# Kernel tuning notes

Measured on AMD Instinct MI355X. Metric: run time of the kernel, lower is better.

## Reference

```python
import jax, jax.numpy as jnp
import numpy as np

N_NODES = 100000
N_EDGES = 1600000
IN_DIM = 128
EMB_DIM = 128
NUM_EDGE_EMB = 4
LN_EPS = 1e-5


def setup_inputs() -> dict:
    key = jax.random.key(0)
    ks = jax.random.split(key, 8)
    x = jax.random.normal(ks[0], (N_NODES, IN_DIM), dtype=jnp.float32)
    edge_index = jax.random.randint(ks[1], (2, N_EDGES), 0, N_NODES, dtype=jnp.int64)
    edge_attr = jax.random.randint(ks[2], (N_EDGES,), 0, NUM_EDGE_EMB, dtype=jnp.int64)
    # learned params
    edge_emb = jax.random.normal(ks[3], (NUM_EDGE_EMB, IN_DIM), dtype=jnp.float32)
    eps = jnp.zeros((), dtype=jnp.float32)  # GINEConv train_eps init 0
    s1 = 1.0 / np.sqrt(IN_DIM)
    W1 = jax.random.uniform(ks[4], (IN_DIM, EMB_DIM), jnp.float32, -s1, s1)
    b1 = jnp.zeros((EMB_DIM,), jnp.float32)
    ln_g = jnp.ones((EMB_DIM,), jnp.float32)
    ln_b = jnp.zeros((EMB_DIM,), jnp.float32)
    s2 = 1.0 / np.sqrt(EMB_DIM)
    W2 = jax.random.uniform(ks[5], (EMB_DIM, EMB_DIM), jnp.float32, -s2, s2)
    b2 = jnp.zeros((EMB_DIM,), jnp.float32)
    return {"x": x, "edge_index": edge_index, "edge_attr": edge_attr,
            "edge_emb": edge_emb, "eps": eps, "W1": W1, "b1": b1,
            "ln_g": ln_g, "ln_b": ln_b, "W2": W2, "b2": b2}


def reference(x, edge_index, edge_attr, edge_emb, eps, W1, b1, ln_g, ln_b, W2, b2):
    src, dst = edge_index[0], edge_index[1]
    # message: relu(x_j + e_ji), gathered per edge [E, D]
    msg = jax.nn.relu(x[src] + edge_emb[edge_attr])
    # scatter-add into destination nodes [N, D]
    agg = jax.ops.segment_sum(msg, dst, num_segments=x.shape[0])
    h = (1.0 + eps) * x + agg
    # MLP: Linear -> LayerNorm -> ReLU -> Linear
    h1 = h @ W1 + b1
    mu = jnp.mean(h1, axis=-1, keepdims=True)
    var = jnp.var(h1, axis=-1, keepdims=True)
    h1 = (h1 - mu) * jax.lax.rsqrt(var + LN_EPS) * ln_g + ln_b
    h1 = jax.nn.relu(h1)
    return h1 @ W2 + b2
```

## Files before the change

### kernel.cpp

```cpp
#include <hip/hip_runtime.h>
#include <hip/hip_fp16.h>

#define N_NODES 100000
#define N_EDGES 1600000
#define DIM 128
#define NBUK 782
#define EPB 4096
#define NBLK 391
#define NCNT (NBUK * NBLK)
#define NSC 299
#define CAPB 2720
#define CAPH 1536
#define EPT 11

typedef __attribute__((ext_vector_type(4))) float f32x4;
typedef _Float16 h2 __attribute__((ext_vector_type(2)));
typedef _Float16 h8v __attribute__((ext_vector_type(8)));

__device__ __forceinline__ unsigned short f2h16(float f) {
    return __half_as_ushort(__float2half(f));
}

__global__ __launch_bounds__(256) void hist2_conv(
    const int* __restrict__ ei, int* __restrict__ cnts,
    const float* __restrict__ x, ushort* __restrict__ xh, int do_conv)
{
    __shared__ int cnt[NBUK];
    for (int i = threadIdx.x; i < NBUK; i += 256) cnt[i] = 0;

    if (do_conv) {
        for (int i = blockIdx.x * 256 + threadIdx.x; i < N_NODES * DIM / 4;
             i += NBLK * 256) {
            float4 v = ((const float4*)x)[i];
            ushort4 o;
            o.x = f2h16(v.x);
            o.y = f2h16(v.y);
            o.z = f2h16(v.z);
            o.w = f2h16(v.w);
            ((ushort4*)xh)[i] = o;
        }
    }
    __syncthreads();

    int e0 = blockIdx.x * EPB;
    int e1 = min(e0 + EPB, N_EDGES);
    for (int e = e0 + threadIdx.x; e < e1; e += 256)
        atomicAdd(&cnt[ei[N_EDGES + e] >> 7], 1);
    __syncthreads();
    for (int b = threadIdx.x; b < NBUK; b += 256)
        cnts[b * NBLK + blockIdx.x] = cnt[b];
}

__global__ __launch_bounds__(256) void scanA(
    int* __restrict__ cnts, int* __restrict__ bsums)
{
    __shared__ int s[256];
    int t = threadIdx.x;
    int base = blockIdx.x * 1024 + t * 4;
    int v0 = (base + 0 < NCNT) ? cnts[base + 0] : 0;
    int v1 = (base + 1 < NCNT) ? cnts[base + 1] : 0;
    int v2 = (base + 2 < NCNT) ? cnts[base + 2] : 0;
    int v3 = (base + 3 < NCNT) ? cnts[base + 3] : 0;
    int sum = v0 + v1 + v2 + v3;
    s[t] = sum;
    __syncthreads();
    for (int off = 1; off < 256; off <<= 1) {
        int x = (t >= off) ? s[t - off] : 0;
        __syncthreads();
        s[t] += x;
        __syncthreads();
    }
    int excl = s[t] - sum;
    if (base + 0 < NCNT) cnts[base + 0] = excl;  excl += v0;
    if (base + 1 < NCNT) cnts[base + 1] = excl;  excl += v1;
    if (base + 2 < NCNT) cnts[base + 2] = excl;  excl += v2;
    if (base + 3 < NCNT) cnts[base + 3] = excl;
    if (t == 255) bsums[blockIdx.x] = s[255];
}

__global__ __launch_bounds__(512) void scanC_prepw(
    int* __restrict__ ebase, const int* __restrict__ bsums, int* __restrict__ bk,
    const float* __restrict__ W1, const float* __restrict__ W2,
    ushort* __restrict__ wf1, ushort* __restrict__ wf2)
{
    __shared__ int s[512];
    __shared__ int ex[512];
    int t = threadIdx.x;
    int v = (t < NSC) ? bsums[t] : 0;
    s[t] = v;
    __syncthreads();
    for (int off = 1; off < 512; off <<= 1) {
        int x = (t >= off) ? s[t - off] : 0;
        __syncthreads();
        s[t] += x;
        __syncthreads();
    }
    ex[t] = s[t] - v;
    __syncthreads();

    int i = blockIdx.x * 512 + t;
    if (i < NCNT) {
        int val = ebase[i] + ex[i >> 10];
        ebase[i] = val;
        if (i % NBLK == 0) bk[i / NBLK] = val;
    }
    if (i == 0) bk[NBUK] = N_EDGES;

    if (i < DIM * DIM) {
        int lane = (i >> 3) & 63;
        int j = i & 7;
        int frag = i >> 9;
        int kt = frag >> 3, nt = frag & 7;
        int k = kt * 32 + (lane >> 4) * 8 + j;
        int n = nt * 16 + (lane & 15);
        wf1[i] = f2h16(W1[k * DIM + n]);
        wf2[i] = f2h16(W2[k * DIM + n]);
    }
}

__global__ __launch_bounds__(256) void pass2_scatter(
    const int* __restrict__ ei, const int* __restrict__ ea,
    const int* __restrict__ ebase, int* __restrict__ ebuf)
{
    __shared__ int cnt[NBUK];
    __shared__ int mybase[NBUK];
    for (int i = threadIdx.x; i < NBUK; i += 256) {
        cnt[i] = 0;
        mybase[i] = ebase[i * NBLK + blockIdx.x];
    }
    __syncthreads();
    int e0 = blockIdx.x * EPB;
    int e1 = min(e0 + EPB, N_EDGES);
    for (int e = e0 + threadIdx.x; e < e1; e += 256) {
        int src = ei[e];
        int dst = ei[N_EDGES + e];
        int at  = ea[e];
        int pay = src | (at << 17) | ((dst & 127) << 19);
        int b   = dst >> 7;
        int r   = atomicAdd(&cnt[b], 1);
        ebuf[mybase[b] + r] = pay;
    }
}

template<int HI>
__device__ __forceinline__ float h2acc(h2 m2, float acc) {
#if __has_builtin(__builtin_amdgcn_fdot2)
    h2 b;
    b[0] = (_Float16)(HI ? 0.f : 1.f);
    b[1] = (_Float16)(HI ? 1.f : 0.f);
    return __builtin_amdgcn_fdot2(m2, b, acc, false);
#else
    return acc + (float)m2[HI];
#endif
}

__device__ __forceinline__ void edge_acc(
    int pkv, int c, const unsigned* embh, float* acc, uint4 xv)
{
    const uint4 ev = *(const uint4*)&embh[((((unsigned)pkv >> 17) & 3) << 6) | (c << 2)];
    unsigned xs[4] = {xv.x, xv.y, xv.z, xv.w};
    unsigned es[4] = {ev.x, ev.y, ev.z, ev.w};
    const h2 z2 = (h2)(_Float16)0;
    #pragma unroll
    for (int j = 0; j < 4; ++j) {
        h2 a = __builtin_bit_cast(h2, xs[j]);
        h2 b = __builtin_bit_cast(h2, es[j]);
        h2 m2 = __builtin_elementwise_max(a + b, z2);
        acc[2 * j]     = h2acc<0>(m2, acc[2 * j]);
        acc[2 * j + 1] = h2acc<1>(m2, acc[2 * j + 1]);
    }
}

template<int USE16>
__global__ __launch_bounds__(256) void sort_gather(
    const int* __restrict__ bk, const int* __restrict__ ebuf,
    const float* __restrict__ x, const ushort* __restrict__ xh,
    const float* __restrict__ emb, const float* __restrict__ eps_p,
    ushort* __restrict__ hb)
{
    __shared__ int col_l[CAPH];
    __shared__ int deg[64], sc[64], cur[64];
    __shared__ unsigned embh[256];
    __shared__ float femb[512];

    const int bb = blockIdx.x;
    const int b = bb >> 1;
    const int half = bb & 1;
    const int t = threadIdx.x;
    const int lo = bk[b];
    const int n_e = min(bk[b + 1] - lo, CAPB);

    {
        float2 f = ((const float2*)emb)[t];
        if (USE16) {
            __half2 h = __floats2half2_rn(f.x, f.y);
            embh[t] = __builtin_bit_cast(unsigned, h);
        } else {
            femb[2 * t] = f.x;
            femb[2 * t + 1] = f.y;
        }
    }
    if (t < 64) deg[t] = 0;
    __syncthreads();

    int er[EPT];
    #pragma unroll
    for (int j = 0; j < EPT; ++j) {
        int i = t + j * 256;
        int pk = (i < n_e) ? ebuf[lo + i] : -1;
        if (pk != -1 && (int)(((unsigned)pk >> 25) & 1) != half) pk = -1;
        er[j] = pk;
    }

    #pragma unroll
    for (int j = 0; j < EPT; ++j)
        if (er[j] != -1)
            atomicAdd(&deg[((unsigned)er[j] >> 19) & 63], 1);
    __syncthreads();

    if (t < 64) sc[t] = deg[t];
    __syncthreads();
    for (int off = 1; off < 64; off <<= 1) {
        int v = 0;
        if (t < 64 && t >= off) v = sc[t - off];
        __syncthreads();
        if (t < 64) sc[t] += v;
        __syncthreads();
    }
    if (t < 64) cur[t] = sc[t] - deg[t];
    __syncthreads();

    #pragma unroll
    for (int j = 0; j < EPT; ++j)
        if (er[j] != -1) {
            int p = atomicAdd(&cur[((unsigned)er[j] >> 19) & 63], 1);
            col_l[p] = er[j];
        }
    __syncthreads();

    const int g = t >> 4, c = t & 15;
    const float epsv = 1.0f + eps_p[0];

    for (int ln = g; ln < 64; ln += 16) {
        int n = b * 128 + half * 64 + ln;
        if (n >= N_NODES) break;
        int start = sc[ln] - deg[ln], end = sc[ln];
        float acc[8] = {0.f, 0.f, 0.f, 0.f, 0.f, 0.f, 0.f, 0.f};

        if (USE16) {
            int p = start;
            for (; p + 4 <= end; p += 4) {
                int pk[4];
                uint4 xv[4];
                #pragma unroll
                for (int u = 0; u < 4; ++u) pk[u] = col_l[p + u];
                #pragma unroll
                for (int u = 0; u < 4; ++u)
                    xv[u] = ((const uint4*)xh)[((pk[u] & 0x1FFFF) << 4) | c];
                #pragma unroll
                for (int u = 0; u < 4; ++u)
                    edge_acc(pk[u], c, embh, acc, xv[u]);
            }
            for (; p < end; ++p) {
                int pkv = col_l[p];
                uint4 xv = ((const uint4*)xh)[((pkv & 0x1FFFF) << 4) | c];
                edge_acc(pkv, c, embh, acc, xv);
            }
        } else {
            for (int p = start; p < end; ++p) {
                int pk = col_l[p];
                const float* xr = x + (size_t)(pk & 0x1FFFF) * DIM;
                float4 xa = ((const float4*)xr)[c * 2];
                float4 xb = ((const float4*)xr)[c * 2 + 1];
                const float* er2 = &femb[(((unsigned)pk >> 17) & 3) * DIM + c * 8];
                acc[0] += fmaxf(xa.x + er2[0], 0.f);
                acc[1] += fmaxf(xa.y + er2[1], 0.f);
                acc[2] += fmaxf(xa.z + er2[2], 0.f);
                acc[3] += fmaxf(xa.w + er2[3], 0.f);
                acc[4] += fmaxf(xb.x + er2[4], 0.f);
                acc[5] += fmaxf(xb.y + er2[5], 0.f);
                acc[6] += fmaxf(xb.z + er2[6], 0.f);
                acc[7] += fmaxf(xb.w + er2[7], 0.f);
            }
        }

        float o[8];
        {
            uint4 xn = ((const uint4*)xh)[((unsigned)n << 4) | c];
            unsigned xs[4] = {xn.x, xn.y, xn.z, xn.w};
            #pragma unroll
            for (int j = 0; j < 4; ++j) {
                h2 a = __builtin_bit_cast(h2, xs[j]);
                o[2 * j]     = epsv * (float)a[0] + acc[2 * j];
                o[2 * j + 1] = epsv * (float)a[1] + acc[2 * j + 1];
            }
        }

        unsigned pw[4];
        #pragma unroll
        for (int j = 0; j < 4; ++j) {
            __half2 hh = __floats2half2_rn(o[2 * j], o[2 * j + 1]);
            pw[j] = __builtin_bit_cast(unsigned, hh);
        }
        ((uint4*)(hb + (size_t)n * DIM))[c] = make_uint4(pw[0], pw[1], pw[2], pw[3]);
    }
}

__global__ __launch_bounds__(256) void fused_mlp(
    const ushort* __restrict__ hb,
    const ushort* __restrict__ wf1, const ushort* __restrict__ wf2,
    const float* __restrict__ b1,
    const float* __restrict__ lng, const float* __restrict__ lnb,
    const float* __restrict__ b2,
    float* __restrict__ out)
{
    __shared__ ushort w1s[DIM * DIM];
    __shared__ ushort w2s[DIM * DIM];
    __shared__ ushort scr[4 * 16 * DIM];

    #pragma unroll
    for (int i = 0; i < 8; ++i) {
        int idx = i * 256 + threadIdx.x;
        ((uint4*)w1s)[idx] = ((const uint4*)wf1)[idx];
        ((uint4*)w2s)[idx] = ((const uint4*)wf2)[idx];
    }
    __syncthreads();

    const int w  = threadIdx.x >> 6;
    const int l  = threadIdx.x & 63;
    const int lc = l & 15;
    const int lr = l >> 4;

    const int rbase = blockIdx.x * 64 + w * 16;
    const int arow = min(rbase + lc, N_NODES - 1);
    const ushort* hp = hb + (size_t)arow * DIM;

    float g[8], bb[8], bi1[8], bi2[8];
    #pragma unroll
    for (int nt = 0; nt < 8; ++nt) {
        g[nt]  = lng[nt * 16 + lc];
        bb[nt] = lnb[nt * 16 + lc];
        bi1[nt] = b1[nt * 16 + lc];
        bi2[nt] = b2[nt * 16 + lc];
    }

    f32x4 acc[8];
    #pragma unroll
    for (int nt = 0; nt < 8; ++nt)
        acc[nt] = (f32x4){bi1[nt], bi1[nt], bi1[nt], bi1[nt]};

    #pragma unroll
    for (int kt = 0; kt < 4; ++kt) {
        h8v a = *(const h8v*)(hp + kt * 32 + lr * 8);
        #pragma unroll
        for (int nt = 0; nt < 8; ++nt) {
            h8v bf = *(const h8v*)&w1s[((kt * 8 + nt) * 64 + l) * 8];
            acc[nt] = __builtin_amdgcn_mfma_f32_16x16x32_f16(a, bf, acc[nt], 0, 0, 0);
        }
    }

    #pragma unroll
    for (int r = 0; r < 4; ++r) {
        float s1 = 0.f, s2 = 0.f;
        #pragma unroll
        for (int nt = 0; nt < 8; ++nt) { float v = acc[nt][r]; s1 += v; s2 += v * v; }
        s1 += __shfl_xor(s1, 1);  s2 += __shfl_xor(s2, 1);
        s1 += __shfl_xor(s1, 2);  s2 += __shfl_xor(s2, 2);
        s1 += __shfl_xor(s1, 4);  s2 += __shfl_xor(s2, 4);
        s1 += __shfl_xor(s1, 8);  s2 += __shfl_xor(s2, 8);
        float mu  = s1 * (1.0f / DIM);
        float var = s2 * (1.0f / DIM) - mu * mu;
        float rsd = rsqrtf(var + 1e-5f);
        int row = lr * 4 + r;
        #pragma unroll
        for (int nt = 0; nt < 8; ++nt) {
            float v = (acc[nt][r] - mu) * rsd * g[nt] + bb[nt];
            v = fmaxf(v, 0.f);
            int cidx = nt * 16 + lc;
            scr[w * 2048 + row * 128 + (((cidx >> 3) ^ row) << 3) + (cidx & 7)]
                = f2h16(v);
        }
    }

    f32x4 acc2[8];
    #pragma unroll
    for (int nt = 0; nt < 8; ++nt)
        acc2[nt] = (f32x4){bi2[nt], bi2[nt], bi2[nt], bi2[nt]};

    #pragma unroll
    for (int kt = 0; kt < 4; ++kt) {
        h8v a2 = *(const h8v*)&scr[w * 2048 + lc * 128 + (((kt * 4 + lr) ^ lc) << 3)];
        #pragma unroll
        for (int nt = 0; nt < 8; ++nt) {
            h8v bf = *(const h8v*)&w2s[((kt * 8 + nt) * 64 + l) * 8];
            acc2[nt] = __builtin_amdgcn_mfma_f32_16x16x32_f16(a2, bf, acc2[nt], 0, 0, 0);
        }
    }

    #pragma unroll
    for (int r = 0; r < 4; ++r) {
        int orow = rbase + lr * 4 + r;
        if (orow < N_NODES) {
            #pragma unroll
            for (int nt = 0; nt < 8; ++nt)
                out[(size_t)orow * DIM + nt * 16 + lc] = acc2[nt][r];
        }
    }
}

extern "C" void kernel_launch(void* const* d_in, const int* in_sizes, int n_in,
                              void* d_out, int out_size, void* d_ws, size_t ws_size,
                              hipStream_t stream) {
    const float* x    = (const float*)d_in[0];
    const int*   ei   = (const int*)d_in[1];
    const int*   ea   = (const int*)d_in[2];
    const float* emb  = (const float*)d_in[3];
    const float* epsp = (const float*)d_in[4];
    const float* W1   = (const float*)d_in[5];
    const float* b1   = (const float*)d_in[6];
    const float* lng  = (const float*)d_in[7];
    const float* lnb  = (const float*)d_in[8];
    const float* W2   = (const float*)d_in[9];
    const float* b2   = (const float*)d_in[10];
    float* out = (float*)d_out;

    char* ws = (char*)d_ws;
    int* bk     = (int*)(ws);
    int* bsums  = (int*)(ws + 4096);
    ushort* wf1 = (ushort*)(ws + 8192);
    ushort* wf2 = (ushort*)(ws + 40960);
    int* cnts   = (int*)(ws + 81920);
    int* ebuf   = (int*)(ws + 1310720);
    ushort* hb  = (ushort*)(ws + 8025984);
    ushort* xh  = (ushort*)(ws + 59225984);
    const size_t NEED = 59225984 + (size_t)N_NODES * DIM * 2;

    const int use_f16 = (ws_size >= NEED) ? 1 : 0;

    hist2_conv<<<NBLK, 256, 0, stream>>>(ei, cnts, x, xh, use_f16);
    scanA<<<NSC, 256, 0, stream>>>(cnts, bsums);
    scanC_prepw<<<(NCNT + 511) / 512, 512, 0, stream>>>(
        cnts, bsums, bk, W1, W2, wf1, wf2);
    pass2_scatter<<<NBLK, 256, 0, stream>>>(ei, ea, cnts, ebuf);

    if (use_f16) {
        sort_gather<1><<<NBUK * 2, 256, 0, stream>>>(
            bk, ebuf, x, xh, emb, epsp, hb);
    } else {
        sort_gather<0><<<NBUK * 2, 256, 0, stream>>>(
            bk, ebuf, x, xh, emb, epsp, hb);
    }

    fused_mlp<<<(N_NODES + 63) / 64, 256, 0, stream>>>(
        hb, wf1, wf2, b1, lng, lnb, b2, out);
}
```

Measured before the change: 140.8 us.

## Fuse CSR-build kernels into one cooperative kernel with grid syncs

Merges the histogram/convert, two scan phases, weight prep and scatter kernels into a single cooperative launch of 391 blocks, using grid.sync between phases instead of separate kernel launches. This removes three launch boundaries and their inter-kernel gaps. In exchange, every block waits at each grid barrier, and every block now redundantly scans the 299 block sums. The second scan phase runs on one 256-thread block shape instead of 512-thread blocks.

```diff
diff --git a/kernel.cpp b/kernel.cpp
--- a/kernel.cpp
+++ b/kernel.cpp
@@ -1,5 +1,8 @@
 #include <hip/hip_runtime.h>
 #include <hip/hip_fp16.h>
+#include <hip/hip_cooperative_groups.h>
+
+namespace cg = cooperative_groups;
 
 #define N_NODES 100000
 #define N_EDGES 1600000
@@ -21,16 +24,27 @@
     return __half_as_ushort(__float2half(f));
 }
 
-__global__ __launch_bounds__(256) void hist2_conv(
-    const int* __restrict__ ei, int* __restrict__ cnts,
-    const float* __restrict__ x, ushort* __restrict__ xh, int do_conv)
+__global__ __launch_bounds__(256) void csr_build(
+    const int* __restrict__ ei, const int* __restrict__ ea,
+    const float* __restrict__ x, ushort* __restrict__ xh,
+    int* __restrict__ cnts, int* __restrict__ bsums, int* __restrict__ bk,
+    const float* __restrict__ W1, const float* __restrict__ W2,
+    ushort* __restrict__ wf1, ushort* __restrict__ wf2,
+    int* __restrict__ ebuf, int use_f16)
 {
+    cg::grid_group grid = cg::this_grid();
+
     __shared__ int cnt[NBUK];
-    for (int i = threadIdx.x; i < NBUK; i += 256) cnt[i] = 0;
-
-    if (do_conv) {
-        for (int i = blockIdx.x * 256 + threadIdx.x; i < N_NODES * DIM / 4;
-             i += NBLK * 256) {
+    __shared__ int mybase[NBUK];
+    __shared__ int sB[512];
+    __shared__ int exB[512];
+
+    const int blk = blockIdx.x;
+    const int t = threadIdx.x;
+
+    for (int i = t; i < NBUK; i += 256) cnt[i] = 0;
+    if (use_f16) {
+        for (int i = blk * 256 + t; i < N_NODES * DIM / 4; i += NBLK * 256) {
             float4 v = ((const float4*)x)[i];
             ushort4 o;
             o.x = f2h16(v.x);
@@ -42,96 +56,84 @@
     }
     __syncthreads();
 
-    int e0 = blockIdx.x * EPB;
+    int e0 = blk * EPB;
     int e1 = min(e0 + EPB, N_EDGES);
-    for (int e = e0 + threadIdx.x; e < e1; e += 256)
+    for (int e = e0 + t; e < e1; e += 256)
         atomicAdd(&cnt[ei[N_EDGES + e] >> 7], 1);
     __syncthreads();
-    for (int b = threadIdx.x; b < NBUK; b += 256)
-        cnts[b * NBLK + blockIdx.x] = cnt[b];
-}
-
-__global__ __launch_bounds__(256) void scanA(
-    int* __restrict__ cnts, int* __restrict__ bsums)
-{
-    __shared__ int s[256];
-    int t = threadIdx.x;
-    int base = blockIdx.x * 1024 + t * 4;
-    int v0 = (base + 0 < NCNT) ? cnts[base + 0] : 0;
-    int v1 = (base + 1 < NCNT) ? cnts[base + 1] : 0;
-    int v2 = (base + 2 < NCNT) ? cnts[base + 2] : 0;
-    int v3 = (base + 3 < NCNT) ? cnts[base + 3] : 0;
-    int sum = v0 + v1 + v2 + v3;
-    s[t] = sum;
-    __syncthreads();
-    for (int off = 1; off < 256; off <<= 1) {
-        int x = (t >= off) ? s[t - off] : 0;
+    for (int b = t; b < NBUK; b += 256)
+        cnts[b * NBLK + blk] = cnt[b];
+
+    grid.sync();
+
+    if (blk < NSC) {
+        int base = blk * 1024 + t * 4;
+        int v0 = (base + 0 < NCNT) ? cnts[base + 0] : 0;
+        int v1 = (base + 1 < NCNT) ? cnts[base + 1] : 0;
+        int v2 = (base + 2 < NCNT) ? cnts[base + 2] : 0;
+        int v3 = (base + 3 < NCNT) ? cnts[base + 3] : 0;
+        int sum = v0 + v1 + v2 + v3;
+        sB[t] = sum;
         __syncthreads();
-        s[t] += x;
+        for (int off = 1; off < 256; off <<= 1) {
+            int xg = (t >= off) ? sB[t - off] : 0;
+            __syncthreads();
+            sB[t] += xg;
+            __syncthreads();
+        }
+        int excl = sB[t] - sum;
+        if (base + 0 < NCNT) cnts[base + 0] = excl;  excl += v0;
+        if (base + 1 < NCNT) cnts[base + 1] = excl;  excl += v1;
+        if (base + 2 < NCNT) cnts[base + 2] = excl;  excl += v2;
+        if (base + 3 < NCNT) cnts[base + 3] = excl;
+        if (t == 255) bsums[blk] = sB[255];
+    }
+
+    grid.sync();
+
+    {
+        int vA = (t < NSC) ? bsums[t] : 0;
+        int vB = (t + 256 < NSC) ? bsums[t + 256] : 0;
+        sB[t] = vA; sB[t + 256] = vB;
         __syncthreads();
-    }
-    int excl = s[t] - sum;
-    if (base + 0 < NCNT) cnts[base + 0] = excl;  excl += v0;
-    if (base + 1 < NCNT) cnts[base + 1] = excl;  excl += v1;
-    if (base + 2 < NCNT) cnts[base + 2] = excl;  excl += v2;
-    if (base + 3 < NCNT) cnts[base + 3] = excl;
-    if (t == 255) bsums[blockIdx.x] = s[255];
-}
-
-__global__ __launch_bounds__(512) void scanC_prepw(
-    int* __restrict__ ebase, const int* __restrict__ bsums, int* __restrict__ bk,
-    const float* __restrict__ W1, const float* __restrict__ W2,
-    ushort* __restrict__ wf1, ushort* __restrict__ wf2)
-{
-    __shared__ int s[512];
-    __shared__ int ex[512];
-    int t = threadIdx.x;
-    int v = (t < NSC) ? bsums[t] : 0;
-    s[t] = v;
-    __syncthreads();
-    for (int off = 1; off < 512; off <<= 1) {
-        int x = (t >= off) ? s[t - off] : 0;
+        for (int off = 1; off < 512; off <<= 1) {
+            int x0 = (t >= off) ? sB[t - off] : 0;
+            int x1 = (t + 256 >= off) ? sB[t + 256 - off] : 0;
+            __syncthreads();
+            sB[t] += x0; sB[t + 256] += x1;
+            __syncthreads();
+        }
+        exB[t] = sB[t] - vA;
+        exB[t + 256] = sB[t + 256] - vB;
         __syncthreads();
-        s[t] += x;
-        __syncthreads();
-    }
-    ex[t] = s[t] - v;
-    __syncthreads();
-
-    int i = blockIdx.x * 512 + t;
-    if (i < NCNT) {
-        int val = ebase[i] + ex[i >> 10];
-        ebase[i] = val;
-        if (i % NBLK == 0) bk[i / NBLK] = val;
-    }
-    if (i == 0) bk[NBUK] = N_EDGES;
-
-    if (i < DIM * DIM) {
-        int lane = (i >> 3) & 63;
-        int j = i & 7;
-        int frag = i >> 9;
-        int kt = frag >> 3, nt = frag & 7;
-        int k = kt * 32 + (lane >> 4) * 8 + j;
-        int n = nt * 16 + (lane & 15);
-        wf1[i] = f2h16(W1[k * DIM + n]);
-        wf2[i] = f2h16(W2[k * DIM + n]);
-    }
-}
-
-__global__ __launch_bounds__(256) void pass2_scatter(
-    const int* __restrict__ ei, const int* __restrict__ ea,
-    const int* __restrict__ ebase, int* __restrict__ ebuf)
-{
-    __shared__ int cnt[NBUK];
-    __shared__ int mybase[NBUK];
-    for (int i = threadIdx.x; i < NBUK; i += 256) {
+
+        for (int i = blk * 256 + t; i < NCNT; i += NBLK * 256) {
+            int val = cnts[i] + exB[i >> 10];
+            cnts[i] = val;
+            if (i % NBLK == 0) bk[i / NBLK] = val;
+        }
+        if (blk == 0 && t == 0) bk[NBUK] = N_EDGES;
+
+        for (int i = blk * 256 + t; i < DIM * DIM; i += NBLK * 256) {
+            int lane = (i >> 3) & 63;
+            int j = i & 7;
+            int frag = i >> 9;
+            int kt = frag >> 3, nt = frag & 7;
+            int k = kt * 32 + (lane >> 4) * 8 + j;
+            int n = nt * 16 + (lane & 15);
+            wf1[i] = f2h16(W1[k * DIM + n]);
+            wf2[i] = f2h16(W2[k * DIM + n]);
+        }
+    }
+
+    grid.sync();
+
+    for (int i = t; i < NBUK; i += 256) {
         cnt[i] = 0;
-        mybase[i] = ebase[i * NBLK + blockIdx.x];
-    }
-    __syncthreads();
-    int e0 = blockIdx.x * EPB;
-    int e1 = min(e0 + EPB, N_EDGES);
-    for (int e = e0 + threadIdx.x; e < e1; e += 256) {
+        mybase[i] = cnts[i * NBLK + blk];
+    }
+    __syncthreads();
+    for (int e = e0 + t; e < e1; e += 256) {
         int src = ei[e];
         int dst = ei[N_EDGES + e];
         int at  = ea[e];
@@ -411,9 +413,9 @@
 extern "C" void kernel_launch(void* const* d_in, const int* in_sizes, int n_in,
                               void* d_out, int out_size, void* d_ws, size_t ws_size,
                               hipStream_t stream) {
-    const float* x    = (const float*)d_in[0];
     const int*   ei   = (const int*)d_in[1];
     const int*   ea   = (const int*)d_in[2];
+    const float* x    = (const float*)d_in[0];
     const float* emb  = (const float*)d_in[3];
     const float* epsp = (const float*)d_in[4];
     const float* W1   = (const float*)d_in[5];
@@ -435,13 +437,16 @@
     ushort* xh  = (ushort*)(ws + 59225984);
     const size_t NEED = 59225984 + (size_t)N_NODES * DIM * 2;
 
-    const int use_f16 = (ws_size >= NEED) ? 1 : 0;
-
-    hist2_conv<<<NBLK, 256, 0, stream>>>(ei, cnts, x, xh, use_f16);
-    scanA<<<NSC, 256, 0, stream>>>(cnts, bsums);
-    scanC_prepw<<<(NCNT + 511) / 512, 512, 0, stream>>>(
-        cnts, bsums, bk, W1, W2, wf1, wf2);
-    pass2_scatter<<<NBLK, 256, 0, stream>>>(ei, ea, cnts, ebuf);
+    int use_f16 = (ws_size >= NEED) ? 1 : 0;
+
+    void* args[] = {
+        (void*)&ei, (void*)&ea, (void*)&x, (void*)&xh,
+        (void*)&cnts, (void*)&bsums, (void*)&bk,
+        (void*)&W1, (void*)&W2, (void*)&wf1, (void*)&wf2,
+        (void*)&ebuf, (void*)&use_f16
+    };
+    hipLaunchCooperativeKernel((const void*)csr_build, dim3(NBLK), dim3(256),
+                               args, 0, stream);
 
     if (use_f16) {
         sort_gather<1><<<NBUK * 2, 256, 0, stream>>>(
```

After: 295.3 us. 2.1x slower.
